# Kernel optimization log

Hardware: AMD Instinct MI355X
Metric: run time of the kernel (lower is better)

Reference implementation:

```python
import jax, jax.numpy as jnp
import numpy as np

EPS = 1e-5
NUM_GROUPS = 32
NUM_HEADS = 4


def setup_inputs() -> dict:
    key = jax.random.key(0)
    ks = jax.random.split(key, 3)
    B, C, H, W = 4, 256, 64, 64
    x = jax.random.normal(ks[0], (B, C, H, W), dtype=jnp.float32)
    gn_w = jnp.ones((C,), jnp.float32)
    gn_b = jnp.zeros((C,), jnp.float32)
    qkv_w = jax.random.normal(ks[1], (3 * C, C), dtype=jnp.float32) * (C ** -0.5)
    qkv_b = jnp.zeros((3 * C,), jnp.float32)
    proj_w = jax.random.normal(ks[2], (C, C), dtype=jnp.float32) * (C ** -0.5)
    proj_b = jnp.zeros((C,), jnp.float32)
    return {"x": x, "gn_w": gn_w, "gn_b": gn_b, "qkv_w": qkv_w,
            "qkv_b": qkv_b, "proj_w": proj_w, "proj_b": proj_b}


def _group_norm(x, w, b):
    B, C, H, W = x.shape
    xg = x.reshape(B, NUM_GROUPS, C // NUM_GROUPS, H, W)
    mean = xg.mean(axis=(2, 3, 4), keepdims=True)
    var = xg.var(axis=(2, 3, 4), keepdims=True)
    xn = ((xg - mean) * jax.lax.rsqrt(var + EPS)).reshape(B, C, H, W)
    return xn * w[None, :, None, None] + b[None, :, None, None]


def reference(x, gn_w, gn_b, qkv_w, qkv_b, proj_w, proj_b):
    B, C, H, W = x.shape
    nh = NUM_HEADS
    d = C // nh
    L = H * W
    h = _group_norm(x, gn_w, gn_b)
    # 1x1 conv == channel matmul
    qkv = jnp.einsum('oc,bchw->bohw', qkv_w, h) + qkv_b[None, :, None, None]
    q, k, v = jnp.split(qkv, 3, axis=1)
    # (B, C, H, W) -> (B, nh, L, d)
    def to_heads(t):
        return t.reshape(B, nh, d, L).transpose(0, 1, 3, 2)
    q, k, v = to_heads(q), to_heads(k), to_heads(v)
    scale = d ** -0.5
    attn = jax.nn.softmax(jnp.einsum('bhqd,bhkd->bhqk', q, k) * scale, axis=-1)
    o = jnp.einsum('bhqk,bhkd->bhqd', attn, v)          # (B, nh, L, d)
    o = o.transpose(0, 1, 3, 2).reshape(B, C, H, W)
    o = jnp.einsum('oc,bchw->bohw', proj_w, o) + proj_b[None, :, None, None]
    return x + o
```

## Files before the change

kernel.cpp:

```cpp
#include <hip/hip_runtime.h>

#define B_   4
#define C_   256
#define L_   4096
#define NH_  4
#define D_   64
#define G_   32
#define CPG_ 8

typedef __bf16 bf16x8 __attribute__((ext_vector_type(8)));
typedef float  f32x4  __attribute__((ext_vector_type(4)));

__device__ __forceinline__ ushort f2bf(float f) {
  union { float f; unsigned u; } c; c.f = f;
  unsigned u = c.u;
  return (ushort)((u + 0x7fffu + ((u >> 16) & 1u)) >> 16);
}
__device__ __forceinline__ float bf2f(ushort h) {
  union { unsigned u; float f; } c; c.u = ((unsigned)h) << 16; return c.f;
}
__device__ __forceinline__ unsigned fbits(float f) {
  union { float f; unsigned u; } c; c.f = f; return c.u;
}
__device__ __forceinline__ float fastexp2(float x) {
#if __has_builtin(__builtin_amdgcn_exp2f)
  return __builtin_amdgcn_exp2f(x);
#else
  return exp2f(x);
#endif
}

__global__ __launch_bounds__(256) void cvt_kernel(const float* __restrict__ wq,
                                                  const float* __restrict__ wp,
                                                  ushort* __restrict__ oq,
                                                  ushort* __restrict__ op,
                                                  float* __restrict__ stats) {
  int t = blockIdx.x * 256 + threadIdx.x;
  if (blockIdx.x == 0) stats[threadIdx.x] = 0.f;
  const int NQ4 = (768 * 256) / 4;
  float4 v;
  if (t < NQ4) {
    v = ((const float4*)wq)[t];
    ((ushort4*)oq)[t] = make_ushort4(f2bf(v.x), f2bf(v.y), f2bf(v.z), f2bf(v.w));
  } else {
    int i = t - NQ4;
    v = ((const float4*)wp)[i];
    ((ushort4*)op)[i] = make_ushort4(f2bf(v.x), f2bf(v.y), f2bf(v.z), f2bf(v.w));
  }
}

__global__ __launch_bounds__(256) void gn_stats(const float* __restrict__ x,
                                                float* __restrict__ stats) {
  int bg = blockIdx.x >> 3, chunk = blockIdx.x & 7;
  int b = bg >> 5, g = bg & 31;
  const float* xg = x + ((size_t)b * C_ + g * CPG_) * L_ + chunk * 512;
  int tid = threadIdx.x;

  float s = 0.f, ss = 0.f;
  for (int c = 0; c < CPG_; ++c) {
    float2 v = ((const float2*)(xg + (size_t)c * L_))[tid];
    s  += v.x + v.y;
    ss += v.x * v.x + v.y * v.y;
  }
  for (int off = 32; off; off >>= 1) { s += __shfl_xor(s, off); ss += __shfl_xor(ss, off); }
  __shared__ float red[8];
  int w = tid >> 6;
  if ((tid & 63) == 0) { red[w] = s; red[4 + w] = ss; }
  __syncthreads();
  if (tid == 0) {
    atomicAdd(&stats[bg * 2],     red[0] + red[1] + red[2] + red[3]);
    atomicAdd(&stats[bg * 2 + 1], red[4] + red[5] + red[6] + red[7]);
  }
}

__global__ __launch_bounds__(256) void gn_apply(const float* __restrict__ x,
                                                const float* __restrict__ gw,
                                                const float* __restrict__ gb,
                                                const float* __restrict__ stats,
                                                ushort* __restrict__ hT) {
  int bg = blockIdx.x >> 3, chunk = blockIdx.x & 7;
  int b = bg >> 5, g = bg & 31;
  const float* xg = x + ((size_t)b * C_ + g * CPG_) * L_;
  int tid = threadIdx.x;

  const float inv_n = 1.0f / (CPG_ * L_);
  float mean = stats[bg * 2] * inv_n;
  float var  = stats[bg * 2 + 1] * inv_n - mean * mean;
  float rstd = rsqrtf(var + 1e-5f);

  float wv[CPG_], bv[CPG_];
  for (int c = 0; c < CPG_; ++c) { wv[c] = gw[g * CPG_ + c]; bv[c] = gb[g * CPG_ + c]; }

  for (int li = 0; li < 2; ++li) {
    int l = chunk * 512 + li * 256 + tid;
    union { ushort s[8]; uint4 u; } o;
    for (int c = 0; c < CPG_; ++c) {
      float v = xg[(size_t)c * L_ + l];
      o.s[c] = f2bf((v - mean) * rstd * wv[c] + bv[c]);
    }
    *(uint4*)(hT + ((size_t)b * L_ + l) * C_ + g * CPG_) = o.u;
  }
}

__global__ __launch_bounds__(256) void qkv_kernel(const ushort* __restrict__ hT,
                                                  const ushort* __restrict__ w,
                                                  const float* __restrict__ bias,
                                                  ushort* __restrict__ q,
                                                  ushort* __restrict__ k,
                                                  ushort* __restrict__ v) {
  int wid  = blockIdx.x * 4 + (threadIdx.x >> 6);
  int lane = threadIdx.x & 63;
  int quad = lane >> 4, col = lane & 15;
  int ot   = wid % 12;
  int rest = wid / 12;
  int lt   = rest & 127;
  int b    = rest >> 7;
  int o0 = ot * 64, l0 = lt * 32;

  const ushort* abase = w  + (size_t)(o0 + col) * C_ + quad * 8;
  const ushort* bbase = hT + ((size_t)b * L_ + l0 + col) * C_ + quad * 8;

  f32x4 acc[4][2];
  for (int i = 0; i < 4; ++i) for (int j = 0; j < 2; ++j)
    acc[i][j] = (f32x4){0.f, 0.f, 0.f, 0.f};

  for (int k0 = 0; k0 < C_; k0 += 32) {
    bf16x8 a[4], bb[2];
#pragma unroll
    for (int i = 0; i < 4; ++i) a[i]  = *(const bf16x8*)(abase + (size_t)(i * 16) * C_ + k0);
#pragma unroll
    for (int j = 0; j < 2; ++j) bb[j] = *(const bf16x8*)(bbase + (size_t)(j * 16) * C_ + k0);
#pragma unroll
    for (int i = 0; i < 4; ++i)
#pragma unroll
      for (int j = 0; j < 2; ++j)
        acc[i][j] = __builtin_amdgcn_mfma_f32_16x16x32_bf16(a[i], bb[j], acc[i][j], 0, 0, 0);
  }

  int third = o0 >> 8;
  int hh    = (o0 & 255) >> 6;
  float scale = (third == 0) ? 0.180336880111120f : 1.0f;
#pragma unroll
  for (int i = 0; i < 4; ++i) {
    int oo = o0 + i * 16 + quad * 4;
    int dd = i * 16 + quad * 4;
#pragma unroll
    for (int j = 0; j < 2; ++j) {
      int l = l0 + j * 16 + col;
      ushort pk[4];
      for (int r = 0; r < 4; ++r) pk[r] = f2bf((acc[i][j][r] + bias[oo + r]) * scale);
      if (third < 2) {
        ushort* dst = (third ? k : q) + (((size_t)(b * NH_ + hh) * L_ + l) * D_ + dd);
        *(ushort4*)dst = make_ushort4(pk[0], pk[1], pk[2], pk[3]);
      } else {
        for (int r = 0; r < 4; ++r)
          v[((size_t)(b * NH_ + hh) * D_ + dd + r) * L_ + l] = pk[r];
      }
    }
  }
}

__global__ __launch_bounds__(256, 4) void attn_kernel(const ushort* __restrict__ q,
                                                      const ushort* __restrict__ k,
                                                      const ushort* __restrict__ v,
                                                      ushort* __restrict__ p0,
                                                      ushort* __restrict__ p1,
                                                      float* __restrict__ psumbuf) {
  __shared__ __align__(16) ushort k_lds[2][64][72];
  __shared__ __align__(16) ushort v_lds[2][64][72];

  int tid   = threadIdx.x;
  int w     = tid >> 6, lane = tid & 63;
  int quad  = lane >> 4, col = lane & 15;
  int split = blockIdx.x >> 9;
  int bh    = (blockIdx.x >> 5) & 15;
  int qblk  = blockIdx.x & 31;

  const ushort* qp = q + (size_t)bh * L_ * D_;
  const ushort* kp = k + (size_t)bh * L_ * D_;
  const ushort* vp = v + (size_t)bh * D_ * L_;

  int qrow0 = qblk * 128 + w * 32;
  bf16x8 bq[2][2];
#pragma unroll
  for (int f = 0; f < 2; ++f)
#pragma unroll
    for (int c = 0; c < 2; ++c)
      bq[f][c] = *(const bf16x8*)(qp + (size_t)(qrow0 + f * 16 + col) * D_ + c * 32 + quad * 8);

  f32x4 oacc[2][4];
#pragma unroll
  for (int f = 0; f < 2; ++f)
    for (int t = 0; t < 4; ++t) oacc[f][t] = (f32x4){0.f, 0.f, 0.f, 0.f};
  f32x4 pacc[2];
  pacc[0] = (f32x4){0.f, 0.f, 0.f, 0.f};
  pacc[1] = (f32x4){0.f, 0.f, 0.f, 0.f};

  union { ushort s[8]; bf16x8 v8; } one_u;
#pragma unroll
  for (int i = 0; i < 8; ++i) one_u.s[i] = 0x3F80;
  bf16x8 ones = one_u.v8;

  int vrow = tid >> 2, vchunk = tid & 3;
  int kt0 = split * (L_ / 2), kt_end = kt0 + L_ / 2;

  {
    const uint4* ksrc = (const uint4*)(kp + (size_t)kt0 * D_);
    uint4 a  = ksrc[tid];
    uint4 b2 = ksrc[tid + 256];
    const uint4* vsrc = (const uint4*)(vp + (size_t)vrow * L_ + kt0);
    uint4 c0 = vsrc[vchunk * 2];
    uint4 c1 = vsrc[vchunk * 2 + 1];
    *(uint4*)&k_lds[0][tid >> 3][(tid & 7) * 8] = a;
    *(uint4*)&k_lds[0][32 + (tid >> 3)][(tid & 7) * 8] = b2;
    *(uint4*)&v_lds[0][vrow][vchunk * 16] = c0;
    *(uint4*)&v_lds[0][vrow][vchunk * 16 + 8] = c1;
  }
  __syncthreads();

  int cur = 0;
  for (int kt = kt0; kt < kt_end; kt += 64) {
    uint4 nk0, nk1, nv0, nv1;
    bool has_next = (kt + 64) < kt_end;
    if (has_next) {
      const uint4* ksrc = (const uint4*)(kp + (size_t)(kt + 64) * D_);
      nk0 = ksrc[tid];
      nk1 = ksrc[tid + 256];
      const uint4* vsrc = (const uint4*)(vp + (size_t)vrow * L_ + (kt + 64));
      nv0 = vsrc[vchunk * 2];
      nv1 = vsrc[vchunk * 2 + 1];
    }

#pragma unroll
    for (int h = 0; h < 2; ++h) {
      f32x4 s0[2], s1[2];
#pragma unroll
      for (int f = 0; f < 2; ++f) { s0[f] = (f32x4){0.f,0.f,0.f,0.f}; s1[f] = (f32x4){0.f,0.f,0.f,0.f}; }
      __builtin_amdgcn_s_setprio(1);
#pragma unroll
      for (int c = 0; c < 2; ++c) {
        bf16x8 a0 = *(const bf16x8*)&k_lds[cur][h * 32 + col][c * 32 + quad * 8];
        bf16x8 a1 = *(const bf16x8*)&k_lds[cur][h * 32 + 16 + col][c * 32 + quad * 8];
#pragma unroll
        for (int f = 0; f < 2; ++f) {
          s0[f] = __builtin_amdgcn_mfma_f32_16x16x32_bf16(a0, bq[f][c], s0[f], 0, 0, 0);
          s1[f] = __builtin_amdgcn_mfma_f32_16x16x32_bf16(a1, bq[f][c], s1[f], 0, 0, 0);
        }
      }
      __builtin_amdgcn_s_setprio(0);

      bf16x8 pb[2];
#pragma unroll
      for (int f = 0; f < 2; ++f) {
        float pe0[4], pe1[4];
#pragma unroll
        for (int r = 0; r < 4; ++r) {
          pe0[r] = fastexp2(s0[f][r]);
          pe1[r] = fastexp2(s1[f][r]);
        }
        union { unsigned u[4]; bf16x8 v8; } pc;
        pc.u[0] = __builtin_amdgcn_perm(fbits(pe0[1]), fbits(pe0[0]), 0x07060302u);
        pc.u[1] = __builtin_amdgcn_perm(fbits(pe0[3]), fbits(pe0[2]), 0x07060302u);
        pc.u[2] = __builtin_amdgcn_perm(fbits(pe1[1]), fbits(pe1[0]), 0x07060302u);
        pc.u[3] = __builtin_amdgcn_perm(fbits(pe1[3]), fbits(pe1[2]), 0x07060302u);
        pb[f] = pc.v8;
      }

      __builtin_amdgcn_s_setprio(1);
#pragma unroll
      for (int f = 0; f < 2; ++f)
        pacc[f] = __builtin_amdgcn_mfma_f32_16x16x32_bf16(ones, pb[f], pacc[f], 0, 0, 0);
#pragma unroll
      for (int t = 0; t < 4; ++t) {
        union { uint2 u2[2]; bf16x8 v8; } vc;
        vc.u2[0] = *(const uint2*)&v_lds[cur][t * 16 + col][h * 32 + quad * 4];
        vc.u2[1] = *(const uint2*)&v_lds[cur][t * 16 + col][h * 32 + 16 + quad * 4];
        bf16x8 av = vc.v8;
#pragma unroll
        for (int f = 0; f < 2; ++f)
          oacc[f][t] = __builtin_amdgcn_mfma_f32_16x16x32_bf16(av, pb[f], oacc[f][t], 0, 0, 0);
      }
      __builtin_amdgcn_s_setprio(0);
    }

    if (has_next) {
      int nb = cur ^ 1;
      *(uint4*)&k_lds[nb][tid >> 3][(tid & 7) * 8] = nk0;
      *(uint4*)&k_lds[nb][32 + (tid >> 3)][(tid & 7) * 8] = nk1;
      *(uint4*)&v_lds[nb][vrow][vchunk * 16] = nv0;
      *(uint4*)&v_lds[nb][vrow][vchunk * 16 + 8] = nv1;
      __syncthreads();
      cur = nb;
    }
  }

  ushort* po = split ? p1 : p0;
#pragma unroll
  for (int f = 0; f < 2; ++f) {
    for (int t = 0; t < 4; ++t) {
      ushort ok[4];
      for (int r = 0; r < 4; ++r) ok[r] = f2bf(oacc[f][t][r]);
      ushort* dst = po + ((size_t)bh * L_ + qrow0 + f * 16 + col) * D_ + t * 16 + quad * 4;
      *(ushort4*)dst = make_ushort4(ok[0], ok[1], ok[2], ok[3]);
    }
    if (quad == 0)
      psumbuf[split * (16 * L_) + bh * L_ + qrow0 + f * 16 + col] = pacc[f][0];
  }
}

__global__ __launch_bounds__(256) void comb_kernel(ushort* __restrict__ p0,
                                                   const ushort* __restrict__ p1,
                                                   const float* __restrict__ ps) {
  int idx = blockIdx.x * 256 + threadIdx.x;
  int row = idx >> 4;
  float inv = 1.0f / (ps[row] + ps[16 * L_ + row]);
  ushort4 a = ((const ushort4*)p0)[idx];
  ushort4 b = ((const ushort4*)p1)[idx];
  ((ushort4*)p0)[idx] = make_ushort4(
      f2bf((bf2f(a.x) + bf2f(b.x)) * inv),
      f2bf((bf2f(a.y) + bf2f(b.y)) * inv),
      f2bf((bf2f(a.z) + bf2f(b.z)) * inv),
      f2bf((bf2f(a.w) + bf2f(b.w)) * inv));
}

__global__ __launch_bounds__(256) void proj_kernel(const ushort* __restrict__ oin,
                                                   const ushort* __restrict__ pw,
                                                   const float* __restrict__ pb,
                                                   const float* __restrict__ x,
                                                   float* __restrict__ out) {
  int wid  = blockIdx.x * 4 + (threadIdx.x >> 6);
  int lane = threadIdx.x & 63;
  int quad = lane >> 4, col = lane & 15;
  int oct  = wid & 7;
  int rest = wid >> 3;
  int lt   = rest & 127;
  int b    = rest >> 7;
  int l0 = lt * 32, oc0 = oct * 32;

  f32x4 acc[2][2];
  for (int i = 0; i < 2; ++i) for (int j = 0; j < 2; ++j)
    acc[i][j] = (f32x4){0.f, 0.f, 0.f, 0.f};

  for (int k0 = 0; k0 < C_; k0 += 32) {
    int hh = k0 >> 6, dk = k0 & 63;
    bf16x8 a[2], bb[2];
#pragma unroll
    for (int i = 0; i < 2; ++i)
      a[i] = *(const bf16x8*)(oin + ((size_t)(b * NH_ + hh) * L_ + l0 + i * 16 + col) * D_ + dk + quad * 8);
#pragma unroll
    for (int j = 0; j < 2; ++j)
      bb[j] = *(const bf16x8*)(pw + (size_t)(oc0 + j * 16 + col) * C_ + k0 + quad * 8);
#pragma unroll
    for (int i = 0; i < 2; ++i)
#pragma unroll
      for (int j = 0; j < 2; ++j)
        acc[i][j] = __builtin_amdgcn_mfma_f32_16x16x32_bf16(a[i], bb[j], acc[i][j], 0, 0, 0);
  }

#pragma unroll
  for (int j = 0; j < 2; ++j) {
    int oc = oc0 + j * 16 + col;
    float bias = pb[oc];
#pragma unroll
    for (int i = 0; i < 2; ++i) {
      int l = l0 + i * 16 + quad * 4;
      size_t off = ((size_t)b * C_ + oc) * L_ + l;
      float4 xv = *(const float4*)(x + off);
      float4 ov = make_float4(acc[i][j][0] + bias + xv.x,
                              acc[i][j][1] + bias + xv.y,
                              acc[i][j][2] + bias + xv.z,
                              acc[i][j][3] + bias + xv.w);
      *(float4*)(out + off) = ov;
    }
  }
}

extern "C" void kernel_launch(void* const* d_in, const int* in_sizes, int n_in,
                              void* d_out, int out_size, void* d_ws, size_t ws_size,
                              hipStream_t stream) {
  const float* x      = (const float*)d_in[0];
  const float* gn_w   = (const float*)d_in[1];
  const float* gn_b   = (const float*)d_in[2];
  const float* qkv_w  = (const float*)d_in[3];
  const float* qkv_b  = (const float*)d_in[4];
  const float* proj_w = (const float*)d_in[5];
  const float* proj_b = (const float*)d_in[6];
  float* out = (float*)d_out;

  const size_t TEN = (size_t)B_ * C_ * L_;
  ushort* ws  = (ushort*)d_ws;
  ushort* q   = ws;
  ushort* k   = ws + TEN;
  ushort* v   = ws + 2 * TEN;
  ushort* oat = ws + 3 * TEN;
  ushort* wq  = ws + 4 * TEN;
  ushort* wp  = wq + 768 * 256;
  float*  stats = (float*)(wp + 256 * 256);
  ushort* hT  = (ushort*)d_out;
  ushort* p1  = (ushort*)d_out + TEN;
  float*  psb = (float*)d_out;

  cvt_kernel <<<256,       256, 0, stream>>>(qkv_w, proj_w, wq, wp, stats);
  gn_stats   <<<1024,      256, 0, stream>>>(x, stats);
  gn_apply   <<<1024,      256, 0, stream>>>(x, gn_w, gn_b, stats, hT);
  qkv_kernel <<<6144 / 4,  256, 0, stream>>>(hT, wq, qkv_b, q, k, v);
  attn_kernel<<<1024,      256, 0, stream>>>(q, k, v, oat, p1, psb);
  comb_kernel<<<4096,      256, 0, stream>>>(oat, p1, psb);
  proj_kernel<<<4096 / 4,  256, 0, stream>>>(oat, wp, proj_b, x, out);
}
```

Baseline: 225.0 us.

## Restructure attention loop: hoist QK MFMAs, permute V LDS layout, remap blocks

```diff
diff --git a/kernel.cpp b/kernel.cpp
--- a/kernel.cpp
+++ b/kernel.cpp
@@ -124,6 +124,7 @@
   for (int i = 0; i < 4; ++i) for (int j = 0; j < 2; ++j)
     acc[i][j] = (f32x4){0.f, 0.f, 0.f, 0.f};
 
+#pragma unroll
   for (int k0 = 0; k0 < C_; k0 += 32) {
     bf16x8 a[4], bb[2];
 #pragma unroll
@@ -172,9 +173,11 @@
   int tid   = threadIdx.x;
   int w     = tid >> 6, lane = tid & 63;
   int quad  = lane >> 4, col = lane & 15;
-  int split = blockIdx.x >> 9;
-  int bh    = (blockIdx.x >> 5) & 15;
-  int qblk  = blockIdx.x & 31;
+  int bid   = (int)blockIdx.x;
+  bid = (bid & 7) * 128 + (bid >> 3);
+  int split = bid >> 9;
+  int bh    = (bid >> 5) & 15;
+  int qblk  = bid & 31;
 
   const ushort* qp = q + (size_t)bh * L_ * D_;
   const ushort* kp = k + (size_t)bh * L_ * D_;
@@ -195,6 +198,7 @@
   f32x4 pacc[2];
   pacc[0] = (f32x4){0.f, 0.f, 0.f, 0.f};
   pacc[1] = (f32x4){0.f, 0.f, 0.f, 0.f};
+  const f32x4 Z = (f32x4){0.f, 0.f, 0.f, 0.f};
 
   union { ushort s[8]; bf16x8 v8; } one_u;
 #pragma unroll
@@ -202,6 +206,7 @@
   bf16x8 ones = one_u.v8;
 
   int vrow = tid >> 2, vchunk = tid & 3;
+  int vwoff = (vchunk >> 1) * 32 + (vchunk & 1) * 4;
   int kt0 = split * (L_ / 2), kt_end = kt0 + L_ / 2;
 
   {
@@ -213,15 +218,35 @@
     uint4 c1 = vsrc[vchunk * 2 + 1];
     *(uint4*)&k_lds[0][tid >> 3][(tid & 7) * 8] = a;
     *(uint4*)&k_lds[0][32 + (tid >> 3)][(tid & 7) * 8] = b2;
-    *(uint4*)&v_lds[0][vrow][vchunk * 16] = c0;
-    *(uint4*)&v_lds[0][vrow][vchunk * 16 + 8] = c1;
+    ushort* vb = &v_lds[0][vrow][vwoff];
+    *(uint2*)(vb + 0)  = make_uint2(c0.x, c0.y);
+    *(uint2*)(vb + 8)  = make_uint2(c0.z, c0.w);
+    *(uint2*)(vb + 16) = make_uint2(c1.x, c1.y);
+    *(uint2*)(vb + 24) = make_uint2(c1.z, c1.w);
   }
   __syncthreads();
 
   int cur = 0;
   for (int kt = kt0; kt < kt_end; kt += 64) {
+    bool has_next = (kt + 64) < kt_end;
+
+    f32x4 s[2][2][2];
+#pragma unroll
+    for (int h = 0; h < 2; ++h) {
+      bf16x8 a00 = *(const bf16x8*)&k_lds[cur][h * 32 + col][quad * 8];
+      bf16x8 a01 = *(const bf16x8*)&k_lds[cur][h * 32 + col][32 + quad * 8];
+      bf16x8 a10 = *(const bf16x8*)&k_lds[cur][h * 32 + 16 + col][quad * 8];
+      bf16x8 a11 = *(const bf16x8*)&k_lds[cur][h * 32 + 16 + col][32 + quad * 8];
+#pragma unroll
+      for (int f = 0; f < 2; ++f) {
+        s[h][f][0] = __builtin_amdgcn_mfma_f32_16x16x32_bf16(a00, bq[f][0], Z, 0, 0, 0);
+        s[h][f][1] = __builtin_amdgcn_mfma_f32_16x16x32_bf16(a10, bq[f][0], Z, 0, 0, 0);
+        s[h][f][0] = __builtin_amdgcn_mfma_f32_16x16x32_bf16(a01, bq[f][1], s[h][f][0], 0, 0, 0);
+        s[h][f][1] = __builtin_amdgcn_mfma_f32_16x16x32_bf16(a11, bq[f][1], s[h][f][1], 0, 0, 0);
+      }
+    }
+
     uint4 nk0, nk1, nv0, nv1;
-    bool has_next = (kt + 64) < kt_end;
     if (has_next) {
       const uint4* ksrc = (const uint4*)(kp + (size_t)(kt + 64) * D_);
       nk0 = ksrc[tid];
@@ -233,30 +258,14 @@
 
 #pragma unroll
     for (int h = 0; h < 2; ++h) {
-      f32x4 s0[2], s1[2];
-#pragma unroll
-      for (int f = 0; f < 2; ++f) { s0[f] = (f32x4){0.f,0.f,0.f,0.f}; s1[f] = (f32x4){0.f,0.f,0.f,0.f}; }
-      __builtin_amdgcn_s_setprio(1);
-#pragma unroll
-      for (int c = 0; c < 2; ++c) {
-        bf16x8 a0 = *(const bf16x8*)&k_lds[cur][h * 32 + col][c * 32 + quad * 8];
-        bf16x8 a1 = *(const bf16x8*)&k_lds[cur][h * 32 + 16 + col][c * 32 + quad * 8];
-#pragma unroll
-        for (int f = 0; f < 2; ++f) {
-          s0[f] = __builtin_amdgcn_mfma_f32_16x16x32_bf16(a0, bq[f][c], s0[f], 0, 0, 0);
-          s1[f] = __builtin_amdgcn_mfma_f32_16x16x32_bf16(a1, bq[f][c], s1[f], 0, 0, 0);
-        }
-      }
-      __builtin_amdgcn_s_setprio(0);
-
       bf16x8 pb[2];
 #pragma unroll
       for (int f = 0; f < 2; ++f) {
         float pe0[4], pe1[4];
 #pragma unroll
         for (int r = 0; r < 4; ++r) {
-          pe0[r] = fastexp2(s0[f][r]);
-          pe1[r] = fastexp2(s1[f][r]);
+          pe0[r] = fastexp2(s[h][f][0][r]);
+          pe1[r] = fastexp2(s[h][f][1][r]);
         }
         union { unsigned u[4]; bf16x8 v8; } pc;
         pc.u[0] = __builtin_amdgcn_perm(fbits(pe0[1]), fbits(pe0[0]), 0x07060302u);
@@ -265,30 +274,27 @@
         pc.u[3] = __builtin_amdgcn_perm(fbits(pe1[3]), fbits(pe1[2]), 0x07060302u);
         pb[f] = pc.v8;
       }
-
-      __builtin_amdgcn_s_setprio(1);
 #pragma unroll
       for (int f = 0; f < 2; ++f)
         pacc[f] = __builtin_amdgcn_mfma_f32_16x16x32_bf16(ones, pb[f], pacc[f], 0, 0, 0);
 #pragma unroll
       for (int t = 0; t < 4; ++t) {
-        union { uint2 u2[2]; bf16x8 v8; } vc;
-        vc.u2[0] = *(const uint2*)&v_lds[cur][t * 16 + col][h * 32 + quad * 4];
-        vc.u2[1] = *(const uint2*)&v_lds[cur][t * 16 + col][h * 32 + 16 + quad * 4];
-        bf16x8 av = vc.v8;
+        bf16x8 av = *(const bf16x8*)&v_lds[cur][t * 16 + col][h * 32 + quad * 8];
 #pragma unroll
         for (int f = 0; f < 2; ++f)
           oacc[f][t] = __builtin_amdgcn_mfma_f32_16x16x32_bf16(av, pb[f], oacc[f][t], 0, 0, 0);
       }
-      __builtin_amdgcn_s_setprio(0);
     }
 
     if (has_next) {
       int nb = cur ^ 1;
       *(uint4*)&k_lds[nb][tid >> 3][(tid & 7) * 8] = nk0;
       *(uint4*)&k_lds[nb][32 + (tid >> 3)][(tid & 7) * 8] = nk1;
-      *(uint4*)&v_lds[nb][vrow][vchunk * 16] = nv0;
-      *(uint4*)&v_lds[nb][vrow][vchunk * 16 + 8] = nv1;
+      ushort* vb = &v_lds[nb][vrow][vwoff];
+      *(uint2*)(vb + 0)  = make_uint2(nv0.x, nv0.y);
+      *(uint2*)(vb + 8)  = make_uint2(nv0.z, nv0.w);
+      *(uint2*)(vb + 16) = make_uint2(nv1.x, nv1.y);
+      *(uint2*)(vb + 24) = make_uint2(nv1.z, nv1.w);
       __syncthreads();
       cur = nb;
     }
@@ -341,6 +347,7 @@
   for (int i = 0; i < 2; ++i) for (int j = 0; j < 2; ++j)
     acc[i][j] = (f32x4){0.f, 0.f, 0.f, 0.f};
 
+#pragma unroll
   for (int k0 = 0; k0 < C_; k0 += 32) {
     int hh = k0 >> 6, dk = k0 & 63;
     bf16x8 a[2], bb[2];
```

Result: no change. 225.2 us (+0.1%).
